# Kernel tuning notes

Hardware: AMD Instinct MI355X
Metric: run time of the kernel (lower is better)

Reference implementation:

```python
import jax, jax.numpy as jnp
import numpy as np

HEADS = 8
DIM_HEAD = 32
SCALE = DIM_HEAD ** -0.5


def setup_inputs() -> dict:
    key = jax.random.key(0)
    ks = jax.random.split(key, 5)
    b, c, H, W = 4, 256, 48, 48
    n = H * W
    hidden = HEADS * DIM_HEAD
    x = jax.random.normal(ks[0], (b, c, H, W), dtype=jnp.float32)
    pos_bias = jax.random.normal(ks[1], (HEADS, n, n), dtype=jnp.float32) * 0.02
    w_qkv = jax.random.normal(ks[2], (hidden * 3, c), dtype=jnp.float32) * (c ** -0.5)
    w_out = jax.random.normal(ks[3], (c, hidden), dtype=jnp.float32) * (hidden ** -0.5)
    b_out = jax.random.normal(ks[4], (c,), dtype=jnp.float32) * 0.01
    return {"x": x, "pos_bias": pos_bias, "w_qkv": w_qkv, "w_out": w_out, "b_out": b_out}


def reference(x, pos_bias, w_qkv, w_out, b_out):
    b, c, H, W = x.shape
    n = H * W
    xf = x.reshape(b, c, n)                                  # [b, c, n]
    qkv = jnp.einsum('oc,bcn->bon', w_qkv, xf)               # 1x1 conv, no bias
    q, k, v = jnp.split(qkv, 3, axis=1)                      # each [b, hidden, n]
    def to_heads(t):
        return t.reshape(b, HEADS, DIM_HEAD, n)              # b h d n
    q, k, v = to_heads(q) * SCALE, to_heads(k), to_heads(v)
    sim = jnp.einsum('bhdi,bhdj->bhij', q, k)                # [b, h, n, n]
    sim = sim + pos_bias[None]                               # broadcast over batch
    attn = jax.nn.softmax(sim, axis=-1)
    out = jnp.einsum('bhij,bhdj->bhid', attn, v)             # [b, h, n, d]
    out = out.transpose(0, 1, 3, 2).reshape(b, HEADS * DIM_HEAD, n)  # b (h d) n
    out = jnp.einsum('oc,bcn->bon', w_out, out) + b_out[None, :, None]
    return out.reshape(b, c, H, W)
```

## Files before the change

### kernel.cpp

```cpp
#include <hip/hip_runtime.h>
#include <stdint.h>
#include <stddef.h>

#define BB 4
#define CC 256
#define NH 8
#define DH 32
#define NN 2304
#define O3 768
#define HID 256
#define QK_SCALE 0.17677669529663687f

typedef __attribute__((ext_vector_type(8))) short short8;
typedef __attribute__((ext_vector_type(4))) float float4v;

__device__ __forceinline__ unsigned short f2bf(float f) {
    union { float f; uint32_t u; } v; v.f = f;
    uint32_t u = v.u;
    return (unsigned short)((u + 0x7FFFu + ((u >> 16) & 1u)) >> 16);
}

__global__ void cast_bf16_kernel(const float* __restrict__ src,
                                 unsigned short* __restrict__ dst, int n) {
    int i = blockIdx.x * 256 + threadIdx.x;
    if (i < n) dst[i] = f2bf(src[i]);
}

__global__ __launch_bounds__(256) void qkv_gemm(const float* __restrict__ x,
                                                const float* __restrict__ wqkv,
                                                float* __restrict__ qkv) {
    const int o0 = blockIdx.x * 64;
    const int n0 = blockIdx.y * 64;
    const int b  = blockIdx.z;
    __shared__ float As[16][68];
    __shared__ float Bs[16][68];
    const int t  = threadIdx.x;
    const int tx = t & 15, ty = t >> 4;
    float acc[4][4] = {};
    const float* xb = x + (size_t)b * CC * NN;

    for (int c0 = 0; c0 < CC; c0 += 16) {
        {
            int row = t >> 2;
            int cc  = (t & 3) * 4;
            float4 w4 = *(const float4*)(wqkv + (size_t)(o0 + row) * CC + c0 + cc);
            As[cc + 0][row] = w4.x; As[cc + 1][row] = w4.y;
            As[cc + 2][row] = w4.z; As[cc + 3][row] = w4.w;
        }
        {
            int row = t >> 4;
            int cc  = (t & 15) * 4;
            float4 x4 = *(const float4*)(xb + (size_t)(c0 + row) * NN + n0 + cc);
            *(float4*)&Bs[row][cc] = x4;
        }
        __syncthreads();
        #pragma unroll
        for (int k = 0; k < 16; ++k) {
            float a[4], bv[4];
            *(float4*)a  = *(const float4*)&As[k][ty * 4];
            *(float4*)bv = *(const float4*)&Bs[k][tx * 4];
            #pragma unroll
            for (int i = 0; i < 4; ++i)
                #pragma unroll
                for (int j = 0; j < 4; ++j)
                    acc[i][j] = fmaf(a[i], bv[j], acc[i][j]);
        }
        __syncthreads();
    }
    float* outp = qkv + (size_t)b * O3 * NN;
    #pragma unroll
    for (int i = 0; i < 4; ++i) {
        int o = o0 + ty * 4 + i;
        *(float4*)(outp + (size_t)o * NN + n0 + tx * 4) = *(float4*)acc[i];
    }
}

__global__ __launch_bounds__(256) void pack_qkv(const float* __restrict__ qkv,
                                                unsigned short* __restrict__ q,
                                                unsigned short* __restrict__ k,
                                                unsigned short* __restrict__ v) {
    const int og = blockIdx.x;
    const int o0 = og * 32;
    const int n0 = blockIdx.y * 64;
    const int b  = blockIdx.z;
    const int which = o0 >> 8;
    const int h = (o0 >> 5) & 7;
    const float* src = qkv + ((size_t)b * O3 + o0) * NN + n0;
    const int t = threadIdx.x;

    if (which == 2) {
        unsigned short* dst = v + (((size_t)b * NH + h) * DH) * NN + n0;
        #pragma unroll
        for (int r = 0; r < 8; ++r) {
            int idx = t + r * 256;
            int d = idx >> 6, i = idx & 63;
            dst[(size_t)d * NN + i] = f2bf(src[(size_t)d * NN + i]);
        }
    } else {
        __shared__ float ls[32][65];
        #pragma unroll
        for (int r = 0; r < 8; ++r) {
            int idx = t + r * 256;
            int d = idx >> 6, i = idx & 63;
            ls[d][i] = src[(size_t)d * NN + i];
        }
        __syncthreads();
        const float scale = (which == 0) ? QK_SCALE : 1.0f;
        unsigned short* dst = (which == 0 ? q : k) + (((size_t)b * NH + h) * NN + n0) * DH;
        #pragma unroll
        for (int r = 0; r < 8; ++r) {
            int idx = t + r * 256;
            int i = idx >> 5, d = idx & 31;
            dst[(size_t)i * DH + d] = f2bf(ls[d][i] * scale);
        }
    }
}

__global__ __launch_bounds__(256) void attn_kernel(const unsigned short* __restrict__ qg,
                                                   const unsigned short* __restrict__ kg,
                                                   const unsigned short* __restrict__ vg,
                                                   const float* __restrict__ bias,
                                                   unsigned short* __restrict__ ao) {
    const int i0   = blockIdx.x * 16;
    const int h    = blockIdx.y;
    const int t    = threadIdx.x;
    const int w    = t >> 6;
    const int lane = t & 63;
    const int l15  = lane & 15;
    const int quad = lane >> 4;

    __shared__ float bs[16][68];
    __shared__ unsigned short ps[4][16][72];

    const size_t bh = (size_t)w * NH + h;
    const unsigned short* qp = qg + bh * NN * DH;
    const unsigned short* kp = kg + bh * NN * DH;
    const unsigned short* vp = vg + bh * DH * NN;

    short8 qf = *(const short8*)(qp + (size_t)(i0 + l15) * DH + quad * 8);

    float4v o0acc = {0.f, 0.f, 0.f, 0.f};
    float4v o1acc = {0.f, 0.f, 0.f, 0.f};
    float4v zero  = {0.f, 0.f, 0.f, 0.f};
    float m_r[4], l_r[4];
    #pragma unroll
    for (int r = 0; r < 4; ++r) { m_r[r] = -1e30f; l_r[r] = 0.f; }

    const float* biasrow = bias + ((size_t)h * NN + i0) * NN;

    for (int jt = 0; jt < NN; jt += 64) {
        {
            int row = t >> 4;
            int col = (t & 15) * 4;
            float4 b4 = *(const float4*)(biasrow + (size_t)row * NN + jt + col);
            bs[row][col] = b4.x; bs[row][col + 1] = b4.y;
            bs[row][col + 2] = b4.z; bs[row][col + 3] = b4.w;
        }
        __syncthreads();

        float4v s[4];
        #pragma unroll
        for (int jj = 0; jj < 4; ++jj) {
            short8 kf = *(const short8*)(kp + (size_t)(jt + jj * 16 + l15) * DH + quad * 8);
            s[jj] = __builtin_amdgcn_mfma_f32_16x16x32_bf16(qf, kf, zero, 0, 0, 0);
        }

        #pragma unroll
        for (int r = 0; r < 4; ++r) {
            int row = quad * 4 + r;
            float v0 = s[0][r] + bs[row][l15];
            float v1 = s[1][r] + bs[row][l15 + 16];
            float v2 = s[2][r] + bs[row][l15 + 32];
            float v3 = s[3][r] + bs[row][l15 + 48];
            float mx = fmaxf(fmaxf(v0, v1), fmaxf(v2, v3));
            #pragma unroll
            for (int off = 1; off < 16; off <<= 1)
                mx = fmaxf(mx, __shfl_xor(mx, off, 64));
            float mnew  = fmaxf(m_r[r], mx);
            float alpha = __expf(m_r[r] - mnew);
            float p0 = __expf(v0 - mnew), p1 = __expf(v1 - mnew);
            float p2 = __expf(v2 - mnew), p3 = __expf(v3 - mnew);
            float rs = p0 + p1 + p2 + p3;
            #pragma unroll
            for (int off = 1; off < 16; off <<= 1)
                rs += __shfl_xor(rs, off, 64);
            l_r[r] = l_r[r] * alpha + rs;
            m_r[r] = mnew;
            o0acc[r] *= alpha;
            o1acc[r] *= alpha;
            ps[w][row][l15]      = f2bf(p0);
            ps[w][row][l15 + 16] = f2bf(p1);
            ps[w][row][l15 + 32] = f2bf(p2);
            ps[w][row][l15 + 48] = f2bf(p3);
        }
        __syncthreads();

        short8 pa0 = *(const short8*)&ps[w][l15][quad * 8];
        short8 pa1 = *(const short8*)&ps[w][l15][32 + quad * 8];
        short8 vf00 = *(const short8*)(vp + (size_t)l15 * NN        + jt + quad * 8);
        short8 vf01 = *(const short8*)(vp + (size_t)l15 * NN        + jt + 32 + quad * 8);
        short8 vf10 = *(const short8*)(vp + (size_t)(l15 + 16) * NN + jt + quad * 8);
        short8 vf11 = *(const short8*)(vp + (size_t)(l15 + 16) * NN + jt + 32 + quad * 8);
        o0acc = __builtin_amdgcn_mfma_f32_16x16x32_bf16(pa0, vf00, o0acc, 0, 0, 0);
        o0acc = __builtin_amdgcn_mfma_f32_16x16x32_bf16(pa1, vf01, o0acc, 0, 0, 0);
        o1acc = __builtin_amdgcn_mfma_f32_16x16x32_bf16(pa0, vf10, o1acc, 0, 0, 0);
        o1acc = __builtin_amdgcn_mfma_f32_16x16x32_bf16(pa1, vf11, o1acc, 0, 0, 0);
        __syncthreads();
    }

    unsigned short* aop = ao + ((size_t)w * NN + i0) * HID + h * DH;
    #pragma unroll
    for (int r = 0; r < 4; ++r) {
        int row = quad * 4 + r;
        float inv = 1.0f / l_r[r];
        aop[(size_t)row * HID + l15]      = f2bf(o0acc[r] * inv);
        aop[(size_t)row * HID + 16 + l15] = f2bf(o1acc[r] * inv);
    }
}

__global__ __launch_bounds__(256) void out_proj(const unsigned short* __restrict__ wob,
                                                const unsigned short* __restrict__ aob,
                                                const float* __restrict__ bout,
                                                float* __restrict__ out) {
    const int n0 = blockIdx.x * 64;
    const int o0 = blockIdx.y * 64;
    const int b  = blockIdx.z;
    const int t = threadIdx.x;
    const int w = t >> 6, lane = t & 63, l15 = lane & 15, quad = lane >> 4;
    const int orow = o0 + w * 16;

    float4v acc[4] = {{0.f,0.f,0.f,0.f},{0.f,0.f,0.f,0.f},
                      {0.f,0.f,0.f,0.f},{0.f,0.f,0.f,0.f}};
    const unsigned short* ap = aob + ((size_t)b * NN + n0) * HID;
    #pragma unroll
    for (int c0 = 0; c0 < HID; c0 += 32) {
        short8 af = *(const short8*)(wob + (size_t)(orow + l15) * HID + c0 + quad * 8);
        #pragma unroll
        for (int jj = 0; jj < 4; ++jj) {
            short8 bf = *(const short8*)(ap + (size_t)(jj * 16 + l15) * HID + c0 + quad * 8);
            acc[jj] = __builtin_amdgcn_mfma_f32_16x16x32_bf16(af, bf, acc[jj], 0, 0, 0);
        }
    }
    float* op = out + (size_t)b * HID * NN;
    #pragma unroll
    for (int r = 0; r < 4; ++r) {
        int o = orow + quad * 4 + r;
        float bv = bout[o];
        #pragma unroll
        for (int jj = 0; jj < 4; ++jj)
            op[(size_t)o * NN + n0 + jj * 16 + l15] = acc[jj][r] + bv;
    }
}

extern "C" void kernel_launch(void* const* d_in, const int* in_sizes, int n_in,
                              void* d_out, int out_size, void* d_ws, size_t ws_size,
                              hipStream_t stream) {
    const float* x        = (const float*)d_in[0];
    const float* pos_bias = (const float*)d_in[1];
    const float* w_qkv    = (const float*)d_in[2];
    const float* w_out    = (const float*)d_in[3];
    const float* b_out    = (const float*)d_in[4];
    float* out = (float*)d_out;

    char* ws = (char*)d_ws;
    float*          qkv = (float*)(ws);
    unsigned short* q   = (unsigned short*)(ws + 28311552);
    unsigned short* k   = (unsigned short*)(ws + 33030144);
    unsigned short* v   = (unsigned short*)(ws + 37748736);
    unsigned short* ao  = (unsigned short*)(ws + 42467328);
    unsigned short* wob = (unsigned short*)(ws + 47185920);

    cast_bf16_kernel<<<(HID * HID + 255) / 256, 256, 0, stream>>>(w_out, wob, HID * HID);
    qkv_gemm<<<dim3(O3 / 64, NN / 64, BB), 256, 0, stream>>>(x, w_qkv, qkv);
    pack_qkv<<<dim3(O3 / 32, NN / 64, BB), 256, 0, stream>>>(qkv, q, k, v);
    attn_kernel<<<dim3(NN / 16, NH), 256, 0, stream>>>(q, k, v, pos_bias, ao);
    out_proj<<<dim3(NN / 64, HID / 64, BB), 256, 0, stream>>>(wob, ao, b_out, out);
}
```

Measured before the change: 490.7 us.

## Use bf16 MFMA QKV projection with split weights and double-buffer attention bias

The FP32 scalar QKV GEMM and the separate pack kernel are replaced by a transpose-and-cast of x to bf16 and an MFMA GEMM. Weights are split into hi/lo bf16 parts to keep extra precision, and Q, K and V are written directly in their head layouts. The attention kernel now processes 128-key tiles and prefetches the next pos_bias tile into a double-buffered LDS slot, which removes one barrier per tile. Quantizing x to bf16 lowers accuracy compared with the FP32 projection.

```diff
diff --git a/kernel.cpp b/kernel.cpp
--- a/kernel.cpp
+++ b/kernel.cpp
@@ -19,99 +19,111 @@
     uint32_t u = v.u;
     return (unsigned short)((u + 0x7FFFu + ((u >> 16) & 1u)) >> 16);
 }
-
-__global__ void cast_bf16_kernel(const float* __restrict__ src,
-                                 unsigned short* __restrict__ dst, int n) {
+__device__ __forceinline__ float bf2f(unsigned short s) {
+    union { uint32_t u; float f; } v; v.u = ((uint32_t)s) << 16;
+    return v.f;
+}
+
+__global__ void cast_weights(const float* __restrict__ wqkv,
+                             const float* __restrict__ wout,
+                             unsigned short* __restrict__ whi,
+                             unsigned short* __restrict__ wlo,
+                             unsigned short* __restrict__ wob) {
     int i = blockIdx.x * 256 + threadIdx.x;
-    if (i < n) dst[i] = f2bf(src[i]);
-}
-
-__global__ __launch_bounds__(256) void qkv_gemm(const float* __restrict__ x,
-                                                const float* __restrict__ wqkv,
-                                                float* __restrict__ qkv) {
-    const int o0 = blockIdx.x * 64;
+    float wv = wqkv[i];
+    unsigned short hi = f2bf(wv);
+    whi[i] = hi;
+    wlo[i] = f2bf(wv - bf2f(hi));
+    if (i < HID * HID) wob[i] = f2bf(wout[i]);
+}
+
+__global__ __launch_bounds__(256) void transpose_x(const float* __restrict__ x,
+                                                   unsigned short* __restrict__ xT) {
+    const int n0 = blockIdx.x * 32, c0 = blockIdx.y * 32, b = blockIdx.z;
+    __shared__ float ls[32][33];
+    const int t = threadIdx.x;
+    {
+        int c = t >> 3, nc = (t & 7) * 4;
+        float4 v4 = *(const float4*)(x + ((size_t)b * CC + c0 + c) * NN + n0 + nc);
+        ls[c][nc] = v4.x; ls[c][nc + 1] = v4.y; ls[c][nc + 2] = v4.z; ls[c][nc + 3] = v4.w;
+    }
+    __syncthreads();
+    {
+        int n = t >> 3, cl = (t & 7) * 4;
+        uint32_t p0 = (uint32_t)f2bf(ls[cl + 0][n]) | ((uint32_t)f2bf(ls[cl + 1][n]) << 16);
+        uint32_t p1 = (uint32_t)f2bf(ls[cl + 2][n]) | ((uint32_t)f2bf(ls[cl + 3][n]) << 16);
+        uint32_t* dst = (uint32_t*)(xT + ((size_t)b * NN + n0 + n) * CC + c0 + cl);
+        dst[0] = p0; dst[1] = p1;
+    }
+}
+
+__global__ __launch_bounds__(256) void qkv_gemm_bf16(const unsigned short* __restrict__ xT,
+                                                     const unsigned short* __restrict__ whi,
+                                                     const unsigned short* __restrict__ wlo,
+                                                     unsigned short* __restrict__ q,
+                                                     unsigned short* __restrict__ k,
+                                                     unsigned short* __restrict__ v) {
+    const int og = blockIdx.x;
     const int n0 = blockIdx.y * 64;
     const int b  = blockIdx.z;
-    __shared__ float As[16][68];
-    __shared__ float Bs[16][68];
-    const int t  = threadIdx.x;
-    const int tx = t & 15, ty = t >> 4;
-    float acc[4][4] = {};
-    const float* xb = x + (size_t)b * CC * NN;
-
-    for (int c0 = 0; c0 < CC; c0 += 16) {
-        {
-            int row = t >> 2;
-            int cc  = (t & 3) * 4;
-            float4 w4 = *(const float4*)(wqkv + (size_t)(o0 + row) * CC + c0 + cc);
-            As[cc + 0][row] = w4.x; As[cc + 1][row] = w4.y;
-            As[cc + 2][row] = w4.z; As[cc + 3][row] = w4.w;
-        }
-        {
-            int row = t >> 4;
-            int cc  = (t & 15) * 4;
-            float4 x4 = *(const float4*)(xb + (size_t)(c0 + row) * NN + n0 + cc);
-            *(float4*)&Bs[row][cc] = x4;
-        }
-        __syncthreads();
-        #pragma unroll
-        for (int k = 0; k < 16; ++k) {
-            float a[4], bv[4];
-            *(float4*)a  = *(const float4*)&As[k][ty * 4];
-            *(float4*)bv = *(const float4*)&Bs[k][tx * 4];
-            #pragma unroll
-            for (int i = 0; i < 4; ++i)
-                #pragma unroll
-                for (int j = 0; j < 4; ++j)
-                    acc[i][j] = fmaf(a[i], bv[j], acc[i][j]);
-        }
-        __syncthreads();
-    }
-    float* outp = qkv + (size_t)b * O3 * NN;
-    #pragma unroll
-    for (int i = 0; i < 4; ++i) {
-        int o = o0 + ty * 4 + i;
-        *(float4*)(outp + (size_t)o * NN + n0 + tx * 4) = *(float4*)acc[i];
-    }
-}
-
-__global__ __launch_bounds__(256) void pack_qkv(const float* __restrict__ qkv,
-                                                unsigned short* __restrict__ q,
-                                                unsigned short* __restrict__ k,
-                                                unsigned short* __restrict__ v) {
-    const int og = blockIdx.x;
-    const int o0 = og * 32;
-    const int n0 = blockIdx.y * 64;
-    const int b  = blockIdx.z;
-    const int which = o0 >> 8;
-    const int h = (o0 >> 5) & 7;
-    const float* src = qkv + ((size_t)b * O3 + o0) * NN + n0;
     const int t = threadIdx.x;
-
-    if (which == 2) {
-        unsigned short* dst = v + (((size_t)b * NH + h) * DH) * NN + n0;
-        #pragma unroll
-        for (int r = 0; r < 8; ++r) {
-            int idx = t + r * 256;
-            int d = idx >> 6, i = idx & 63;
-            dst[(size_t)d * NN + i] = f2bf(src[(size_t)d * NN + i]);
+    const int w = t >> 6, lane = t & 63, l15 = lane & 15, quad = lane >> 4;
+    const unsigned short* xb = xT + (size_t)b * NN * CC;
+
+    float4v acc[4] = {{0.f,0.f,0.f,0.f},{0.f,0.f,0.f,0.f},
+                      {0.f,0.f,0.f,0.f},{0.f,0.f,0.f,0.f}};
+
+    if (og < 8) {
+        const int o0 = og * 64;
+        const unsigned short* ap = xb + (size_t)(n0 + w * 16 + l15) * CC + quad * 8;
+        #pragma unroll
+        for (int c0 = 0; c0 < CC; c0 += 32) {
+            short8 af = *(const short8*)(ap + c0);
+            #pragma unroll
+            for (int jj = 0; jj < 4; ++jj) {
+                const size_t wo = (size_t)(o0 + jj * 16 + l15) * CC + c0 + quad * 8;
+                short8 bh = *(const short8*)(whi + wo);
+                short8 bl = *(const short8*)(wlo + wo);
+                acc[jj] = __builtin_amdgcn_mfma_f32_16x16x32_bf16(af, bh, acc[jj], 0, 0, 0);
+                acc[jj] = __builtin_amdgcn_mfma_f32_16x16x32_bf16(af, bl, acc[jj], 0, 0, 0);
+            }
+        }
+        #pragma unroll
+        for (int jj = 0; jj < 4; ++jj) {
+            const int o = o0 + jj * 16 + l15;
+            const int which = o >> 8;
+            const int h = (o >> 5) & 7, d = o & 31;
+            unsigned short* dst = which ? k : q;
+            const float sc = which ? 1.0f : QK_SCALE;
+            #pragma unroll
+            for (int r = 0; r < 4; ++r) {
+                const int n = n0 + w * 16 + quad * 4 + r;
+                dst[(((size_t)b * NH + h) * NN + n) * DH + d] = f2bf(acc[jj][r] * sc);
+            }
         }
     } else {
-        __shared__ float ls[32][65];
-        #pragma unroll
-        for (int r = 0; r < 8; ++r) {
-            int idx = t + r * 256;
-            int d = idx >> 6, i = idx & 63;
-            ls[d][i] = src[(size_t)d * NN + i];
-        }
-        __syncthreads();
-        const float scale = (which == 0) ? QK_SCALE : 1.0f;
-        unsigned short* dst = (which == 0 ? q : k) + (((size_t)b * NH + h) * NN + n0) * DH;
-        #pragma unroll
-        for (int r = 0; r < 8; ++r) {
-            int idx = t + r * 256;
-            int i = idx >> 5, d = idx & 31;
-            dst[(size_t)i * DH + d] = f2bf(ls[d][i] * scale);
+        const int o0 = 512 + (og - 8) * 64;
+        const size_t wr = (size_t)(o0 + w * 16 + l15) * CC + quad * 8;
+        #pragma unroll
+        for (int c0 = 0; c0 < CC; c0 += 32) {
+            short8 ah = *(const short8*)(whi + wr + c0);
+            short8 al = *(const short8*)(wlo + wr + c0);
+            #pragma unroll
+            for (int jj = 0; jj < 4; ++jj) {
+                short8 bf = *(const short8*)(xb + (size_t)(n0 + jj * 16 + l15) * CC + c0 + quad * 8);
+                acc[jj] = __builtin_amdgcn_mfma_f32_16x16x32_bf16(ah, bf, acc[jj], 0, 0, 0);
+                acc[jj] = __builtin_amdgcn_mfma_f32_16x16x32_bf16(al, bf, acc[jj], 0, 0, 0);
+            }
+        }
+        #pragma unroll
+        for (int r = 0; r < 4; ++r) {
+            const int o = o0 + w * 16 + quad * 4 + r;
+            const int h = (o >> 5) & 7, d = o & 31;
+            #pragma unroll
+            for (int jj = 0; jj < 4; ++jj) {
+                const int n = n0 + jj * 16 + l15;
+                v[(((size_t)b * NH + h) * DH + d) * NN + n] = f2bf(acc[jj][r]);
+            }
         }
     }
 }
@@ -129,8 +141,8 @@
     const int l15  = lane & 15;
     const int quad = lane >> 4;
 
-    __shared__ float bs[16][68];
-    __shared__ unsigned short ps[4][16][72];
+    __shared__ float bs[2][16][132];
+    __shared__ unsigned short ps[4][16][136];
 
     const size_t bh = (size_t)w * NH + h;
     const unsigned short* qp = qg + bh * NN * DH;
@@ -139,82 +151,98 @@
 
     short8 qf = *(const short8*)(qp + (size_t)(i0 + l15) * DH + quad * 8);
 
-    float4v o0acc = {0.f, 0.f, 0.f, 0.f};
-    float4v o1acc = {0.f, 0.f, 0.f, 0.f};
-    float4v zero  = {0.f, 0.f, 0.f, 0.f};
+    float4v oa0 = {0.f, 0.f, 0.f, 0.f};
+    float4v oa1 = {0.f, 0.f, 0.f, 0.f};
+    float4v zero = {0.f, 0.f, 0.f, 0.f};
     float m_r[4], l_r[4];
     #pragma unroll
     for (int r = 0; r < 4; ++r) { m_r[r] = -1e30f; l_r[r] = 0.f; }
 
-    const float* biasrow = bias + ((size_t)h * NN + i0) * NN;
-
-    for (int jt = 0; jt < NN; jt += 64) {
-        {
-            int row = t >> 4;
-            int col = (t & 15) * 4;
-            float4 b4 = *(const float4*)(biasrow + (size_t)row * NN + jt + col);
-            bs[row][col] = b4.x; bs[row][col + 1] = b4.y;
-            bs[row][col + 2] = b4.z; bs[row][col + 3] = b4.w;
-        }
-        __syncthreads();
-
-        float4v s[4];
-        #pragma unroll
-        for (int jj = 0; jj < 4; ++jj) {
+    const float* bp = bias + ((size_t)h * NN + i0) * NN;
+    const int brow = t >> 4;
+    const int bcol = (t & 15) * 8;
+
+    {
+        const float* src = bp + (size_t)brow * NN + bcol;
+        float4 f0 = *(const float4*)src;
+        float4 f1 = *(const float4*)(src + 4);
+        *(float4*)&bs[0][brow][bcol]     = f0;
+        *(float4*)&bs[0][brow][bcol + 4] = f1;
+    }
+    __syncthreads();
+
+    for (int it = 0; it < NN / 128; ++it) {
+        const int jt  = it * 128;
+        const int buf = it & 1;
+        const bool pre = (it + 1 < NN / 128);
+        float4 nf0, nf1;
+        if (pre) {
+            const float* src = bp + (size_t)brow * NN + jt + 128 + bcol;
+            nf0 = *(const float4*)src;
+            nf1 = *(const float4*)(src + 4);
+        }
+
+        float4v s[8];
+        #pragma unroll
+        for (int jj = 0; jj < 8; ++jj) {
             short8 kf = *(const short8*)(kp + (size_t)(jt + jj * 16 + l15) * DH + quad * 8);
             s[jj] = __builtin_amdgcn_mfma_f32_16x16x32_bf16(qf, kf, zero, 0, 0, 0);
         }
 
         #pragma unroll
         for (int r = 0; r < 4; ++r) {
-            int row = quad * 4 + r;
-            float v0 = s[0][r] + bs[row][l15];
-            float v1 = s[1][r] + bs[row][l15 + 16];
-            float v2 = s[2][r] + bs[row][l15 + 32];
-            float v3 = s[3][r] + bs[row][l15 + 48];
-            float mx = fmaxf(fmaxf(v0, v1), fmaxf(v2, v3));
+            const int row = quad * 4 + r;
+            float vv[8];
+            #pragma unroll
+            for (int jj = 0; jj < 8; ++jj)
+                vv[jj] = s[jj][r] + bs[buf][row][jj * 16 + l15];
+            float mx = vv[0];
+            #pragma unroll
+            for (int jj = 1; jj < 8; ++jj) mx = fmaxf(mx, vv[jj]);
             #pragma unroll
             for (int off = 1; off < 16; off <<= 1)
                 mx = fmaxf(mx, __shfl_xor(mx, off, 64));
-            float mnew  = fmaxf(m_r[r], mx);
-            float alpha = __expf(m_r[r] - mnew);
-            float p0 = __expf(v0 - mnew), p1 = __expf(v1 - mnew);
-            float p2 = __expf(v2 - mnew), p3 = __expf(v3 - mnew);
-            float rs = p0 + p1 + p2 + p3;
+            const float mnew  = fmaxf(m_r[r], mx);
+            const float alpha = __expf(m_r[r] - mnew);
+            float rs = 0.f;
+            #pragma unroll
+            for (int jj = 0; jj < 8; ++jj) {
+                float p = __expf(vv[jj] - mnew);
+                rs += p;
+                ps[w][row][jj * 16 + l15] = f2bf(p);
+            }
             #pragma unroll
             for (int off = 1; off < 16; off <<= 1)
                 rs += __shfl_xor(rs, off, 64);
             l_r[r] = l_r[r] * alpha + rs;
             m_r[r] = mnew;
-            o0acc[r] *= alpha;
-            o1acc[r] *= alpha;
-            ps[w][row][l15]      = f2bf(p0);
-            ps[w][row][l15 + 16] = f2bf(p1);
-            ps[w][row][l15 + 32] = f2bf(p2);
-            ps[w][row][l15 + 48] = f2bf(p3);
-        }
-        __syncthreads();
-
-        short8 pa0 = *(const short8*)&ps[w][l15][quad * 8];
-        short8 pa1 = *(const short8*)&ps[w][l15][32 + quad * 8];
-        short8 vf00 = *(const short8*)(vp + (size_t)l15 * NN        + jt + quad * 8);
-        short8 vf01 = *(const short8*)(vp + (size_t)l15 * NN        + jt + 32 + quad * 8);
-        short8 vf10 = *(const short8*)(vp + (size_t)(l15 + 16) * NN + jt + quad * 8);
-        short8 vf11 = *(const short8*)(vp + (size_t)(l15 + 16) * NN + jt + 32 + quad * 8);
-        o0acc = __builtin_amdgcn_mfma_f32_16x16x32_bf16(pa0, vf00, o0acc, 0, 0, 0);
-        o0acc = __builtin_amdgcn_mfma_f32_16x16x32_bf16(pa1, vf01, o0acc, 0, 0, 0);
-        o1acc = __builtin_amdgcn_mfma_f32_16x16x32_bf16(pa0, vf10, o1acc, 0, 0, 0);
-        o1acc = __builtin_amdgcn_mfma_f32_16x16x32_bf16(pa1, vf11, o1acc, 0, 0, 0);
+            oa0[r] *= alpha;
+            oa1[r] *= alpha;
+        }
+
+        #pragma unroll
+        for (int c = 0; c < 4; ++c) {
+            short8 pa = *(const short8*)&ps[w][l15][c * 32 + quad * 8];
+            short8 v0 = *(const short8*)(vp + (size_t)l15 * NN        + jt + c * 32 + quad * 8);
+            short8 v1 = *(const short8*)(vp + (size_t)(l15 + 16) * NN + jt + c * 32 + quad * 8);
+            oa0 = __builtin_amdgcn_mfma_f32_16x16x32_bf16(pa, v0, oa0, 0, 0, 0);
+            oa1 = __builtin_amdgcn_mfma_f32_16x16x32_bf16(pa, v1, oa1, 0, 0, 0);
+        }
+
+        if (pre) {
+            *(float4*)&bs[buf ^ 1][brow][bcol]     = nf0;
+            *(float4*)&bs[buf ^ 1][brow][bcol + 4] = nf1;
+        }
         __syncthreads();
     }
 
     unsigned short* aop = ao + ((size_t)w * NN + i0) * HID + h * DH;
     #pragma unroll
     for (int r = 0; r < 4; ++r) {
-        int row = quad * 4 + r;
-        float inv = 1.0f / l_r[r];
-        aop[(size_t)row * HID + l15]      = f2bf(o0acc[r] * inv);
-        aop[(size_t)row * HID + 16 + l15] = f2bf(o1acc[r] * inv);
+        const int row = quad * 4 + r;
+        const float inv = 1.0f / l_r[r];
+        aop[(size_t)row * HID + l15]      = f2bf(oa0[r] * inv);
+        aop[(size_t)row * HID + 16 + l15] = f2bf(oa1[r] * inv);
     }
 }
 
@@ -244,8 +272,8 @@
     float* op = out + (size_t)b * HID * NN;
     #pragma unroll
     for (int r = 0; r < 4; ++r) {
-        int o = orow + quad * 4 + r;
-        float bv = bout[o];
+        const int o = orow + quad * 4 + r;
+        const float bv = bout[o];
         #pragma unroll
         for (int jj = 0; jj < 4; ++jj)
             op[(size_t)o * NN + n0 + jj * 16 + l15] = acc[jj][r] + bv;
@@ -263,16 +291,18 @@
     float* out = (float*)d_out;
 
     char* ws = (char*)d_ws;
-    float*          qkv = (float*)(ws);
-    unsigned short* q   = (unsigned short*)(ws + 28311552);
-    unsigned short* k   = (unsigned short*)(ws + 33030144);
-    unsigned short* v   = (unsigned short*)(ws + 37748736);
-    unsigned short* ao  = (unsigned short*)(ws + 42467328);
-    unsigned short* wob = (unsigned short*)(ws + 47185920);
-
-    cast_bf16_kernel<<<(HID * HID + 255) / 256, 256, 0, stream>>>(w_out, wob, HID * HID);
-    qkv_gemm<<<dim3(O3 / 64, NN / 64, BB), 256, 0, stream>>>(x, w_qkv, qkv);
-    pack_qkv<<<dim3(O3 / 32, NN / 64, BB), 256, 0, stream>>>(qkv, q, k, v);
+    unsigned short* xT  = (unsigned short*)(ws);
+    unsigned short* q   = (unsigned short*)(ws + 4718592);
+    unsigned short* k   = (unsigned short*)(ws + 9437184);
+    unsigned short* v   = (unsigned short*)(ws + 14155776);
+    unsigned short* ao  = (unsigned short*)(ws + 18874368);
+    unsigned short* wob = (unsigned short*)(ws + 23592960);
+    unsigned short* whi = (unsigned short*)(ws + 23724032);
+    unsigned short* wlo = (unsigned short*)(ws + 24117248);
+
+    cast_weights<<<O3 * CC / 256, 256, 0, stream>>>(w_qkv, w_out, whi, wlo, wob);
+    transpose_x<<<dim3(NN / 32, CC / 32, BB), 256, 0, stream>>>(x, xT);
+    qkv_gemm_bf16<<<dim3(12, NN / 64, BB), 256, 0, stream>>>(xT, whi, wlo, q, k, v);
     attn_kernel<<<dim3(NN / 16, NH), 256, 0, stream>>>(q, k, v, pos_bias, ao);
     out_proj<<<dim3(NN / 64, HID / 64, BB), 256, 0, stream>>>(wob, ao, b_out, out);
 }
```

After: 474.4 us. 1.03x faster.
